# Optimization experiments

Hardware: AMD Instinct MI355X
Metric: run time of the kernel (lower is better)

The kernel has to match this reference:

```python
import jax, jax.numpy as jnp
import numpy as np

EPS = 1e-5


def setup_inputs() -> dict:
    key = jax.random.key(0)
    ks = jax.random.split(key, 8)
    B, C, D, H, O, E = 256, 64, 256, 4096, 256, 4
    x = jax.random.normal(ks[0], (B, C, D), dtype=jnp.float32)
    mask_ids = jax.random.randint(ks[1], (B, C), 0, 16)
    projection_idx = jax.random.randint(ks[2], (C,), 0, E)
    W1 = jax.random.normal(ks[3], (E, D, H), dtype=jnp.float32) * 0.02
    b1 = jnp.zeros((E, H), dtype=jnp.float32)
    gamma = jnp.ones((E, H), dtype=jnp.float32)
    beta = jnp.zeros((E, H), dtype=jnp.float32)
    W2 = jax.random.normal(ks[4], (E, H, O), dtype=jnp.float32) * 0.02
    b2 = jnp.zeros((E, O), dtype=jnp.float32)
    return {"x": x, "mask_ids": mask_ids, "projection_idx": projection_idx,
            "W1": W1, "b1": b1, "gamma": gamma, "beta": beta, "W2": W2, "b2": b2}


def reference(x, mask_ids, projection_idx, W1, b1, gamma, beta, W2, b2):
    # x: [B, C, D]; projection_idx: [C] routes each channel to one of E experts.
    # Disjoint masks => the original zeros + masked '+=' is a partition-assign.
    B, C, D = x.shape
    E, _, H = W1.shape
    # Per-channel expert params (gather once, shared over batch).
    h = jnp.einsum('bcd,cdh->bch', x, W1[projection_idx]) + b1[projection_idx]
    # BatchNorm1d in training mode: batch stats over the tokens of each expert
    # (the original flattens the selected [B, |mask|] tokens for BN).
    seg = jnp.broadcast_to(projection_idx[None, :], (B, C)).reshape(-1)  # [B*C]
    hf = h.reshape(B * C, H)
    cnt = jax.ops.segment_sum(jnp.ones((B * C,), h.dtype), seg, num_segments=E)
    cnt = jnp.maximum(cnt, 1.0)
    s1 = jax.ops.segment_sum(hf, seg, num_segments=E)            # [E, H]
    s2 = jax.ops.segment_sum(hf * hf, seg, num_segments=E)       # [E, H]
    mean = s1 / cnt[:, None]
    var = s2 / cnt[:, None] - mean * mean                        # biased var (train-mode BN)
    inv = jax.lax.rsqrt(var + EPS)
    hn = (h - mean[projection_idx]) * (inv[projection_idx] * gamma[projection_idx]) + beta[projection_idx]
    a = jax.nn.relu(hn)
    out = jnp.einsum('bch,cho->bco', a, W2[projection_idx]) + b2[projection_idx]
    return out, mask_ids
```

## Files before the change

kernel.cpp:

```cpp
#include <hip/hip_runtime.h>

typedef unsigned short u16;
typedef unsigned int   u32;
typedef __attribute__((ext_vector_type(8))) short s16x8;
typedef __attribute__((ext_vector_type(4))) float f32x4;
typedef __attribute__((ext_vector_type(4))) u32   u32x4;

#define DEV static __device__ __forceinline__

static constexpr int B_ = 256, C_ = 64, D_ = 256, H_ = 4096, O_ = 256, E_ = 4;

DEV u16 f2bf(float f) {
  u32 u = __builtin_bit_cast(u32, f);
  u += 0x7fffu + ((u >> 16) & 1u);
  return (u16)(u >> 16);
}
DEV float bf2f(u16 u) { return __builtin_bit_cast(float, (u32)u << 16); }

DEV void async16(const u16* g, u16* l) {
  __builtin_amdgcn_global_load_lds(
      (const __attribute__((address_space(1))) void*)g,
      (__attribute__((address_space(3))) void*)l, 16, 0, 0);
}

DEV int xcd_swz(int bid, int nwg) { return (bid & 7) * (nwg >> 3) + (bid >> 3); }

__global__ void k_cvt(const float* __restrict__ src, u16* __restrict__ dst) {
  const int i = blockIdx.x * blockDim.x + threadIdx.x;
  const f32x4 a = ((const f32x4*)src)[2 * i];
  const f32x4 b = ((const f32x4*)src)[2 * i + 1];
  u32x4 o;
  o[0] = (u32)f2bf(a[0]) | ((u32)f2bf(a[1]) << 16);
  o[1] = (u32)f2bf(a[2]) | ((u32)f2bf(a[3]) << 16);
  o[2] = (u32)f2bf(b[0]) | ((u32)f2bf(b[1]) << 16);
  o[3] = (u32)f2bf(b[2]) | ((u32)f2bf(b[3]) << 16);
  ((u32x4*)dst)[i] = o;
}

__global__ void k_transpose(const float* __restrict__ src, u16* __restrict__ dst,
                            const int R, const int Cc) {
  __shared__ float tile[64][65];
  const int nct = Cc >> 6, nrt = R >> 6;
  int bx = blockIdx.x;
  const int ct = bx % nct; bx /= nct;
  const int rt = bx % nrt; const int e = bx / nrt;
  const float* s = src + (size_t)e * R * Cc;
  u16* d = dst + (size_t)e * R * Cc;
  const int tx = threadIdx.x & 63, ty = threadIdx.x >> 6;
  #pragma unroll
  for (int i = 0; i < 64; i += 4)
    tile[i + ty][tx] = s[(size_t)(rt * 64 + i + ty) * Cc + ct * 64 + tx];
  __syncthreads();
  #pragma unroll
  for (int i = 0; i < 64; i += 4) {
    const int cc = i + ty;
    d[(size_t)(ct * 64 + cc) * R + rt * 64 + tx] = f2bf(tile[tx][cc]);
  }
}

__global__ void k_sortc(const int* __restrict__ proj, int* __restrict__ perm) {
  const int c = threadIdx.x;
  const int e = proj[c];
  int rank = 0;
  for (int c2 = 0; c2 < C_; ++c2) {
    const int e2 = proj[c2];
    rank += (e2 < e) || (e2 == e && c2 < c);
  }
  perm[rank] = c;
}

__global__ __launch_bounds__(256, 4)
void k_gemm1(const u16* __restrict__ A, const u16* __restrict__ Bw,
             const int* __restrict__ proj, const int* __restrict__ perm,
             const float* __restrict__ bias,
             u16* __restrict__ outH, float* __restrict__ s1g, float* __restrict__ s2g) {
  constexpr int BM = 128, BN = 128, BK = 32, KT = D_ / BK;
  constexpr int SA = BM * BK / 8, SB = BN * BK / 8;
  constexpr int BUF = (SA + SB) * 8;
  __shared__ __align__(16) u16 lds[2 * BUF];
  const int tid = threadIdx.x, l = tid & 63, w = tid >> 6, wm = w >> 1, wn = w & 1;

  int bid = xcd_swz(blockIdx.x, gridDim.x);
  constexpr int NT = H_ / BN, BT = B_ / BM;
  const int nt = bid % NT; bid /= NT;
  const int bt = bid % BT; const int ci = bid / BT;
  const int c = perm[ci];
  const int e = proj[c];

  const size_t rsA = (size_t)C_ * D_;
  const u16* Ab = A + (size_t)c * D_ + (size_t)bt * BM * rsA;
  const u16* Bb = Bw + ((size_t)e * H_ + (size_t)nt * BN) * D_;

  f32x4 acc[4][4] = {};

  auto stage = [&](int kt) {
    const int k0 = kt * BK;
    u16* dst = lds + (kt & 1) * BUF;
    #pragma unroll
    for (int i = 0; i < 2; ++i) {
      const int s = i * 256 + tid, row = s >> 2, j = (s & 3) ^ (row & 3);
      async16(Ab + (size_t)row * rsA + k0 + j * 8, dst + s * 8);
    }
    #pragma unroll
    for (int i = 0; i < 2; ++i) {
      const int s = i * 256 + tid, col = s >> 2, j = (s & 3) ^ (col & 3);
      async16(Bb + (size_t)col * D_ + k0 + j * 8, dst + SA * 8 + s * 8);
    }
  };

  stage(0);
  asm volatile("s_waitcnt vmcnt(0)" ::: "memory");
  __builtin_amdgcn_s_barrier();

  #pragma unroll
  for (int kt = 0; kt < KT; ++kt) {
    if (kt + 1 < KT) stage(kt + 1);
    const u16* bufA = lds + (kt & 1) * BUF;
    const u16* bufB = bufA + SA * 8;
    s16x8 av[4], bv[4];
    #pragma unroll
    for (int m = 0; m < 4; ++m) {
      const int r = wm * 64 + m * 16 + (l & 15), p = (l >> 4) ^ (r & 3);
      av[m] = *(const s16x8*)(bufA + (r * 4 + p) * 8);
    }
    #pragma unroll
    for (int n = 0; n < 4; ++n) {
      const int cc = wn * 64 + n * 16 + (l & 15), p = (l >> 4) ^ (cc & 3);
      bv[n] = *(const s16x8*)(bufB + (cc * 4 + p) * 8);
    }
    #pragma unroll
    for (int m = 0; m < 4; ++m)
      #pragma unroll
      for (int n = 0; n < 4; ++n)
        acc[m][n] = __builtin_amdgcn_mfma_f32_16x16x32_bf16(av[m], bv[n], acc[m][n], 0, 0, 0);
    asm volatile("s_waitcnt vmcnt(0) lgkmcnt(0)" ::: "memory");
    __builtin_amdgcn_s_barrier();
  }

  u16* ldsOut = lds;
  #pragma unroll
  for (int n = 0; n < 4; ++n) {
    const int colL = wn * 64 + n * 16 + (l & 15);
    const int colg = nt * BN + colL;
    const float bval = bias[e * H_ + colg];
    float p1 = 0.f, p2 = 0.f;
    #pragma unroll
    for (int m = 0; m < 4; ++m) {
      const int rbase = wm * 64 + m * 16 + (l >> 4) * 4;
      #pragma unroll
      for (int i = 0; i < 4; ++i) {
        const float v = acc[m][n][i] + bval;
        p1 += v; p2 += v * v;
        const int row = rbase + i;
        const int phys = (colL >> 3) ^ (row & 15);
        ldsOut[row * 128 + phys * 8 + (colL & 7)] = f2bf(v);
      }
    }
    p1 += __shfl_xor(p1, 16); p1 += __shfl_xor(p1, 32);
    p2 += __shfl_xor(p2, 16); p2 += __shfl_xor(p2, 32);
    if (l < 16) {
      atomicAdd(&s1g[e * H_ + colg], p1);
      atomicAdd(&s2g[e * H_ + colg], p2);
    }
  }
  __syncthreads();
  u16* outB = outH + ((size_t)(bt * BM) * C_ + c) * H_ + nt * BN;
  #pragma unroll
  for (int pass = 0; pass < 8; ++pass) {
    const int row = pass * 16 + (tid >> 4), sl = tid & 15;
    const u32x4 v = *(const u32x4*)(ldsOut + row * 128 + ((sl ^ (row & 15)) * 8));
    *(u32x4*)(outB + (size_t)row * C_ * H_ + sl * 8) = v;
  }
}

__global__ void k_finalize(const float* __restrict__ s1, const float* __restrict__ s2,
                           const int* __restrict__ proj, const float* __restrict__ gamma,
                           const float* __restrict__ beta,
                           u16* __restrict__ sclB, u16* __restrict__ shfB) {
  const int i = blockIdx.x * 256 + threadIdx.x;
  const int e = i >> 12;
  int cn = 0;
  #pragma unroll
  for (int c = 0; c < C_; ++c) cn += (proj[c] == e) ? 1 : 0;
  const float cnt = fmaxf((float)cn * (float)B_, 1.f);
  const float mean = s1[i] / cnt;
  const float var = s2[i] / cnt - mean * mean;
  const float sc = rsqrtf(var + 1e-5f) * gamma[i];
  sclB[i] = f2bf(sc);
  shfB[i] = f2bf(beta[i] - mean * sc);
}

__global__ __launch_bounds__(256, 2)
void k_gemm2(const u16* __restrict__ A, const u16* __restrict__ Bw,
             const int* __restrict__ proj, const int* __restrict__ perm,
             const float* __restrict__ b2,
             const u16* __restrict__ scB, const u16* __restrict__ shB,
             float* __restrict__ outF, float* __restrict__ partial) {
  constexpr int BM = 128, BN = 128, BK = 32, KH = H_ / 2, KT = KH / BK;
  constexpr int SA = BM * BK / 8, SB = BN * BK / 8;
  constexpr int BUF = (SA + SB) * 8;
  __shared__ __align__(16) u16 lds[3 * BUF + 2 * KH];
  u16* stS = lds + 3 * BUF;
  u16* stT = stS + KH;
  const int tid = threadIdx.x, l = tid & 63, w = tid >> 6, wm = w >> 1, wn = w & 1;

  int bid = xcd_swz(blockIdx.x, gridDim.x);
  const int ks = bid & 1; bid >>= 1;
  const int nt = bid & 1; bid >>= 1;
  const int bt = bid & 1; const int ci = bid >> 1;
  const int c = perm[ci];
  const int e = proj[c];

  const size_t rsA = (size_t)C_ * H_;
  const u16* Ab = A + (size_t)c * H_ + (size_t)bt * BM * rsA + (size_t)ks * KH;
  const u16* Bb = Bw + ((size_t)e * O_ + (size_t)nt * BN) * H_ + (size_t)ks * KH;
  const u16* scE = scB + e * H_ + ks * KH;
  const u16* shE = shB + e * H_ + ks * KH;

  f32x4 acc[4][4] = {};
  s16x8 h0[2], h1[2], b0r[2], b1r[2];

  auto Aissue = [&](int kt, s16x8 (&hs)[2]) {
    const int k0 = kt * BK;
    #pragma unroll
    for (int i = 0; i < 2; ++i) {
      const int s = i * 256 + tid, row = s >> 2, j = (s & 3) ^ (row & 3);
      hs[i] = *(const s16x8*)(Ab + (size_t)row * rsA + k0 + j * 8);
    }
  };
  auto Bissue = [&](int kt, s16x8 (&bs)[2]) {
    const int k0 = kt * BK;
    #pragma unroll
    for (int i = 0; i < 2; ++i) {
      const int s = i * 256 + tid, col = s >> 2, j = (s & 3) ^ (col & 3);
      bs[i] = *(const s16x8*)(Bb + (size_t)col * H_ + k0 + j * 8);
    }
  };
  auto Awrite = [&](int kt, s16x8 (&hs)[2]) {
    u16* dst = lds + (kt % 3) * BUF;
    const int k0 = kt * BK;
    #pragma unroll
    for (int i = 0; i < 2; ++i) {
      const int s = i * 256 + tid, row = s >> 2, j = (s & 3) ^ (row & 3);
      const s16x8 sv = *(const s16x8*)(stS + k0 + j * 8);
      const s16x8 tv = *(const s16x8*)(stT + k0 + j * 8);
      u32x4 o;
      #pragma unroll
      for (int jj = 0; jj < 4; ++jj) {
        const float v0 = fmaxf(bf2f((u16)hs[i][2 * jj]) * bf2f((u16)sv[2 * jj]) + bf2f((u16)tv[2 * jj]), 0.f);
        const float v1 = fmaxf(bf2f((u16)hs[i][2 * jj + 1]) * bf2f((u16)sv[2 * jj + 1]) + bf2f((u16)tv[2 * jj + 1]), 0.f);
        o[jj] = (u32)f2bf(v0) | ((u32)f2bf(v1) << 16);
      }
      *(u32x4*)(dst + s * 8) = o;
    }
  };
  auto Bwrite = [&](int kt, s16x8 (&bs)[2]) {
    u16* dst = lds + (kt % 3) * BUF + SA * 8;
    #pragma unroll
    for (int i = 0; i < 2; ++i) {
      const int s = i * 256 + tid;
      *(u32x4*)(dst + s * 8) = __builtin_bit_cast(u32x4, bs[i]);
    }
  };
  auto Compute = [&](int kt) {
    const u16* bufA = lds + (kt % 3) * BUF;
    const u16* bufB = bufA + SA * 8;
    s16x8 av[4], bv[4];
    #pragma unroll
    for (int m = 0; m < 4; ++m) {
      const int r = wm * 64 + m * 16 + (l & 15), p = (l >> 4) ^ (r & 3);
      av[m] = *(const s16x8*)(bufA + (r * 4 + p) * 8);
    }
    #pragma unroll
    for (int n = 0; n < 4; ++n) {
      const int cc = wn * 64 + n * 16 + (l & 15), p = (l >> 4) ^ (cc & 3);
      bv[n] = *(const s16x8*)(bufB + (cc * 4 + p) * 8);
    }
    #pragma unroll
    for (int m = 0; m < 4; ++m)
      #pragma unroll
      for (int n = 0; n < 4; ++n)
        acc[m][n] = __builtin_amdgcn_mfma_f32_16x16x32_bf16(av[m], bv[n], acc[m][n], 0, 0, 0);
  };

  async16(scE + tid * 8, stS + tid * 8);
  async16(shE + tid * 8, stT + tid * 8);
  Aissue(0, h0); Bissue(0, b0r);
  Aissue(1, h1); Bissue(1, b1r);
  asm volatile("s_waitcnt vmcnt(0)" ::: "memory");
  Awrite(0, h0); Bwrite(0, b0r);
  asm volatile("s_waitcnt lgkmcnt(0)" ::: "memory");
  __builtin_amdgcn_s_barrier();

  #pragma unroll 1
  for (int kt = 0; kt + 3 < KT; kt += 2) {
    Aissue(kt + 2, h0); Bissue(kt + 2, b0r);
    Awrite(kt + 1, h1); Bwrite(kt + 1, b1r);
    Compute(kt);
    asm volatile("s_waitcnt lgkmcnt(0)" ::: "memory");
    __builtin_amdgcn_s_barrier();
    Aissue(kt + 3, h1); Bissue(kt + 3, b1r);
    Awrite(kt + 2, h0); Bwrite(kt + 2, b0r);
    Compute(kt + 1);
    asm volatile("s_waitcnt lgkmcnt(0)" ::: "memory");
    __builtin_amdgcn_s_barrier();
  }

  Awrite(KT - 1, h1); Bwrite(KT - 1, b1r);
  Compute(KT - 2);
  asm volatile("s_waitcnt lgkmcnt(0)" ::: "memory");
  __builtin_amdgcn_s_barrier();
  Compute(KT - 1);

  float* dstF = ks ? partial : outF;
  #pragma unroll
  for (int n = 0; n < 4; ++n) {
    const int colg = nt * BN + wn * 64 + n * 16 + (l & 15);
    const float bval = ks ? 0.f : b2[e * O_ + colg];
    #pragma unroll
    for (int m = 0; m < 4; ++m) {
      #pragma unroll
      for (int i = 0; i < 4; ++i) {
        const int rg = bt * BM + wm * 64 + m * 16 + (l >> 4) * 4 + i;
        dstF[((size_t)rg * C_ + c) * O_ + colg] = acc[m][n][i] + bval;
      }
    }
  }
}

__global__ void k_combine(float* __restrict__ out, const float* __restrict__ partial,
                          const int* __restrict__ mask, float* __restrict__ maskOut) {
  const int gi = blockIdx.x * 256 + threadIdx.x;
  const size_t b = (size_t)gi * 2;
  f32x4 a0 = ((const f32x4*)out)[b],     a1 = ((const f32x4*)out)[b + 1];
  const f32x4 p0 = ((const f32x4*)partial)[b], p1 = ((const f32x4*)partial)[b + 1];
  #pragma unroll
  for (int j = 0; j < 4; ++j) { a0[j] += p0[j]; a1[j] += p1[j]; }
  ((f32x4*)out)[b] = a0; ((f32x4*)out)[b + 1] = a1;
  if (gi < B_ * C_ / 8) {
    #pragma unroll
    for (int j = 0; j < 8; ++j) maskOut[gi * 8 + j] = (float)mask[gi * 8 + j];
  }
}

extern "C" void kernel_launch(void* const* d_in, const int* in_sizes, int n_in,
                              void* d_out, int out_size, void* d_ws, size_t ws_size,
                              hipStream_t stream) {
  const float* x     = (const float*)d_in[0];
  const int*   mask  = (const int*)d_in[1];
  const int*   proj  = (const int*)d_in[2];
  const float* W1    = (const float*)d_in[3];
  const float* b1    = (const float*)d_in[4];
  const float* gamma = (const float*)d_in[5];
  const float* beta  = (const float*)d_in[6];
  const float* W2    = (const float*)d_in[7];
  const float* b2    = (const float*)d_in[8];
  float* out = (float*)d_out;

  char* ws = (char*)d_ws;
  size_t off = 0;
  u16* hbuf = (u16*)(ws + off); off += (size_t)B_ * C_ * H_ * 2;
  u16* xb   = (u16*)(ws + off); off += (size_t)B_ * C_ * D_ * 2;
  u16* w1t  = (u16*)(ws + off); off += (size_t)E_ * D_ * H_ * 2;
  float* partial = (float*)xb;
  u16* w2t  = (u16*)(ws + off); off += (size_t)E_ * H_ * O_ * 2;
  float* s1 = (float*)(ws + off); off += (size_t)E_ * H_ * 4;
  float* s2 = (float*)(ws + off); off += (size_t)E_ * H_ * 4;
  u16* sclB = (u16*)(ws + off); off += (size_t)E_ * H_ * 2;
  u16* shfB = (u16*)(ws + off); off += (size_t)E_ * H_ * 2;
  int* perm = (int*)(ws + off); off += 256;

  (void)hipMemsetAsync(s1, 0, (size_t)2 * E_ * H_ * 4, stream);

  k_sortc<<<1, 64, 0, stream>>>(proj, perm);
  k_cvt<<<2048, 256, 0, stream>>>(x, xb);
  k_transpose<<<E_ * 4 * 64, 256, 0, stream>>>(W1, w1t, D_, H_);
  k_transpose<<<E_ * 64 * 4, 256, 0, stream>>>(W2, w2t, H_, O_);

  k_gemm1<<<C_ * 2 * 32, 256, 0, stream>>>(xb, w1t, proj, perm, b1, hbuf, s1, s2);

  k_finalize<<<E_ * H_ / 256, 256, 0, stream>>>(s1, s2, proj, gamma, beta, sclB, shfB);

  k_gemm2<<<512, 256, 0, stream>>>(hbuf, w2t, proj, perm, b2, sclB, shfB, out, partial);

  k_combine<<<B_ * C_ * O_ / 8 / 256, 256, 0, stream>>>(out, partial, mask,
                                                        out + (size_t)B_ * C_ * O_);
}
```

Baseline: 160.1 us.

## Fuse prep kernels, split GEMM2 K four ways, double-buffer and reswizzle LDS

Merges the x conversion, both weight transposes and the channel sort into one prep launch, which removes three launches. GEMM2 gets a templated K-split. When the workspace is large enough it runs with four K slices over 1024 blocks instead of two over 512, with triple buffering cut to double buffering and launch bounds raised for occupancy. Compute is moved ahead of the LDS writes in the pipeline, and the LDS XOR swizzle changes to use row>>1 in both GEMMs. The cost is more partial-sum traffic, since the combine kernel now reads three fp32 partial buffers.

```diff
diff --git a/kernel.cpp b/kernel.cpp
--- a/kernel.cpp
+++ b/kernel.cpp
@@ -25,48 +25,57 @@
 
 DEV int xcd_swz(int bid, int nwg) { return (bid & 7) * (nwg >> 3) + (bid >> 3); }
 
-__global__ void k_cvt(const float* __restrict__ src, u16* __restrict__ dst) {
-  const int i = blockIdx.x * blockDim.x + threadIdx.x;
-  const f32x4 a = ((const f32x4*)src)[2 * i];
-  const f32x4 b = ((const f32x4*)src)[2 * i + 1];
-  u32x4 o;
-  o[0] = (u32)f2bf(a[0]) | ((u32)f2bf(a[1]) << 16);
-  o[1] = (u32)f2bf(a[2]) | ((u32)f2bf(a[3]) << 16);
-  o[2] = (u32)f2bf(b[0]) | ((u32)f2bf(b[1]) << 16);
-  o[3] = (u32)f2bf(b[2]) | ((u32)f2bf(b[3]) << 16);
-  ((u32x4*)dst)[i] = o;
-}
-
-__global__ void k_transpose(const float* __restrict__ src, u16* __restrict__ dst,
-                            const int R, const int Cc) {
+__global__ void k_prep(const float* __restrict__ x, u16* __restrict__ xb,
+                       const float* __restrict__ W1, u16* __restrict__ w1t,
+                       const float* __restrict__ W2, u16* __restrict__ w2t,
+                       const int* __restrict__ proj, int* __restrict__ perm) {
   __shared__ float tile[64][65];
-  const int nct = Cc >> 6, nrt = R >> 6;
-  int bx = blockIdx.x;
-  const int ct = bx % nct; bx /= nct;
-  const int rt = bx % nrt; const int e = bx / nrt;
-  const float* s = src + (size_t)e * R * Cc;
-  u16* d = dst + (size_t)e * R * Cc;
-  const int tx = threadIdx.x & 63, ty = threadIdx.x >> 6;
-  #pragma unroll
-  for (int i = 0; i < 64; i += 4)
-    tile[i + ty][tx] = s[(size_t)(rt * 64 + i + ty) * Cc + ct * 64 + tx];
-  __syncthreads();
-  #pragma unroll
-  for (int i = 0; i < 64; i += 4) {
-    const int cc = i + ty;
-    d[(size_t)(ct * 64 + cc) * R + rt * 64 + tx] = f2bf(tile[tx][cc]);
-  }
-}
-
-__global__ void k_sortc(const int* __restrict__ proj, int* __restrict__ perm) {
-  const int c = threadIdx.x;
-  const int e = proj[c];
-  int rank = 0;
-  for (int c2 = 0; c2 < C_; ++c2) {
-    const int e2 = proj[c2];
-    rank += (e2 < e) || (e2 == e && c2 < c);
-  }
-  perm[rank] = c;
+  const int bx = blockIdx.x, tid = threadIdx.x;
+  if (bx < 2048) {
+    const int i = bx * 256 + tid;
+    const f32x4 a = ((const f32x4*)x)[2 * i];
+    const f32x4 b = ((const f32x4*)x)[2 * i + 1];
+    u32x4 o;
+    o[0] = (u32)f2bf(a[0]) | ((u32)f2bf(a[1]) << 16);
+    o[1] = (u32)f2bf(a[2]) | ((u32)f2bf(a[3]) << 16);
+    o[2] = (u32)f2bf(b[0]) | ((u32)f2bf(b[1]) << 16);
+    o[3] = (u32)f2bf(b[2]) | ((u32)f2bf(b[3]) << 16);
+    ((u32x4*)xb)[i] = o;
+    return;
+  }
+  if (bx < 4096) {
+    const bool w1 = bx < 3072;
+    const int R  = w1 ? D_ : H_;
+    const int Cc = w1 ? H_ : O_;
+    const float* s0 = w1 ? W1 : W2;
+    u16* d0 = w1 ? w1t : w2t;
+    int b = bx - (w1 ? 2048 : 3072);
+    const int nct = Cc >> 6, nrt = R >> 6;
+    const int ct = b % nct; b /= nct;
+    const int rt = b % nrt; const int e = b / nrt;
+    const float* s = s0 + (size_t)e * R * Cc;
+    u16* d = d0 + (size_t)e * R * Cc;
+    const int tx = tid & 63, ty = tid >> 6;
+    #pragma unroll
+    for (int i = 0; i < 64; i += 4)
+      tile[i + ty][tx] = s[(size_t)(rt * 64 + i + ty) * Cc + ct * 64 + tx];
+    __syncthreads();
+    #pragma unroll
+    for (int i = 0; i < 64; i += 4) {
+      const int cc = i + ty;
+      d[(size_t)(ct * 64 + cc) * R + rt * 64 + tx] = f2bf(tile[tx][cc]);
+    }
+    return;
+  }
+  if (tid < C_) {
+    const int e = proj[tid];
+    int rank = 0;
+    for (int c2 = 0; c2 < C_; ++c2) {
+      const int e2 = proj[c2];
+      rank += (e2 < e) || (e2 == e && c2 < tid);
+    }
+    perm[rank] = tid;
+  }
 }
 
 __global__ __launch_bounds__(256, 4)
@@ -98,12 +107,12 @@
     u16* dst = lds + (kt & 1) * BUF;
     #pragma unroll
     for (int i = 0; i < 2; ++i) {
-      const int s = i * 256 + tid, row = s >> 2, j = (s & 3) ^ (row & 3);
+      const int s = i * 256 + tid, row = s >> 2, j = (s & 3) ^ ((row >> 1) & 3);
       async16(Ab + (size_t)row * rsA + k0 + j * 8, dst + s * 8);
     }
     #pragma unroll
     for (int i = 0; i < 2; ++i) {
-      const int s = i * 256 + tid, col = s >> 2, j = (s & 3) ^ (col & 3);
+      const int s = i * 256 + tid, col = s >> 2, j = (s & 3) ^ ((col >> 1) & 3);
       async16(Bb + (size_t)col * D_ + k0 + j * 8, dst + SA * 8 + s * 8);
     }
   };
@@ -120,12 +129,12 @@
     s16x8 av[4], bv[4];
     #pragma unroll
     for (int m = 0; m < 4; ++m) {
-      const int r = wm * 64 + m * 16 + (l & 15), p = (l >> 4) ^ (r & 3);
+      const int r = wm * 64 + m * 16 + (l & 15), p = (l >> 4) ^ ((r >> 1) & 3);
       av[m] = *(const s16x8*)(bufA + (r * 4 + p) * 8);
     }
     #pragma unroll
     for (int n = 0; n < 4; ++n) {
-      const int cc = wn * 64 + n * 16 + (l & 15), p = (l >> 4) ^ (cc & 3);
+      const int cc = wn * 64 + n * 16 + (l & 15), p = (l >> 4) ^ ((cc >> 1) & 3);
       bv[n] = *(const s16x8*)(bufB + (cc * 4 + p) * 8);
     }
     #pragma unroll
@@ -190,22 +199,23 @@
   shfB[i] = f2bf(beta[i] - mean * sc);
 }
 
-__global__ __launch_bounds__(256, 2)
+template<int KS>
+__global__ __launch_bounds__(256, 4)
 void k_gemm2(const u16* __restrict__ A, const u16* __restrict__ Bw,
              const int* __restrict__ proj, const int* __restrict__ perm,
              const float* __restrict__ b2,
              const u16* __restrict__ scB, const u16* __restrict__ shB,
              float* __restrict__ outF, float* __restrict__ partial) {
-  constexpr int BM = 128, BN = 128, BK = 32, KH = H_ / 2, KT = KH / BK;
+  constexpr int BM = 128, BN = 128, BK = 32, KH = H_ / KS, KT = KH / BK;
   constexpr int SA = BM * BK / 8, SB = BN * BK / 8;
   constexpr int BUF = (SA + SB) * 8;
-  __shared__ __align__(16) u16 lds[3 * BUF + 2 * KH];
-  u16* stS = lds + 3 * BUF;
+  __shared__ __align__(16) u16 lds[2 * BUF + 2 * KH];
+  u16* stS = lds + 2 * BUF;
   u16* stT = stS + KH;
   const int tid = threadIdx.x, l = tid & 63, w = tid >> 6, wm = w >> 1, wn = w & 1;
 
   int bid = xcd_swz(blockIdx.x, gridDim.x);
-  const int ks = bid & 1; bid >>= 1;
+  const int ks = bid & (KS - 1); bid /= KS;
   const int nt = bid & 1; bid >>= 1;
   const int bt = bid & 1; const int ci = bid >> 1;
   const int c = perm[ci];
@@ -224,7 +234,7 @@
     const int k0 = kt * BK;
     #pragma unroll
     for (int i = 0; i < 2; ++i) {
-      const int s = i * 256 + tid, row = s >> 2, j = (s & 3) ^ (row & 3);
+      const int s = i * 256 + tid, row = s >> 2, j = (s & 3) ^ ((row >> 1) & 3);
       hs[i] = *(const s16x8*)(Ab + (size_t)row * rsA + k0 + j * 8);
     }
   };
@@ -232,16 +242,16 @@
     const int k0 = kt * BK;
     #pragma unroll
     for (int i = 0; i < 2; ++i) {
-      const int s = i * 256 + tid, col = s >> 2, j = (s & 3) ^ (col & 3);
+      const int s = i * 256 + tid, col = s >> 2, j = (s & 3) ^ ((col >> 1) & 3);
       bs[i] = *(const s16x8*)(Bb + (size_t)col * H_ + k0 + j * 8);
     }
   };
   auto Awrite = [&](int kt, s16x8 (&hs)[2]) {
-    u16* dst = lds + (kt % 3) * BUF;
+    u16* dst = lds + (kt & 1) * BUF;
     const int k0 = kt * BK;
     #pragma unroll
     for (int i = 0; i < 2; ++i) {
-      const int s = i * 256 + tid, row = s >> 2, j = (s & 3) ^ (row & 3);
+      const int s = i * 256 + tid, row = s >> 2, j = (s & 3) ^ ((row >> 1) & 3);
       const s16x8 sv = *(const s16x8*)(stS + k0 + j * 8);
       const s16x8 tv = *(const s16x8*)(stT + k0 + j * 8);
       u32x4 o;
@@ -255,7 +265,7 @@
     }
   };
   auto Bwrite = [&](int kt, s16x8 (&bs)[2]) {
-    u16* dst = lds + (kt % 3) * BUF + SA * 8;
+    u16* dst = lds + (kt & 1) * BUF + SA * 8;
     #pragma unroll
     for (int i = 0; i < 2; ++i) {
       const int s = i * 256 + tid;
@@ -263,17 +273,17 @@
     }
   };
   auto Compute = [&](int kt) {
-    const u16* bufA = lds + (kt % 3) * BUF;
+    const u16* bufA = lds + (kt & 1) * BUF;
     const u16* bufB = bufA + SA * 8;
     s16x8 av[4], bv[4];
     #pragma unroll
     for (int m = 0; m < 4; ++m) {
-      const int r = wm * 64 + m * 16 + (l & 15), p = (l >> 4) ^ (r & 3);
+      const int r = wm * 64 + m * 16 + (l & 15), p = (l >> 4) ^ ((r >> 1) & 3);
       av[m] = *(const s16x8*)(bufA + (r * 4 + p) * 8);
     }
     #pragma unroll
     for (int n = 0; n < 4; ++n) {
-      const int cc = wn * 64 + n * 16 + (l & 15), p = (l >> 4) ^ (cc & 3);
+      const int cc = wn * 64 + n * 16 + (l & 15), p = (l >> 4) ^ ((cc >> 1) & 3);
       bv[n] = *(const s16x8*)(bufB + (cc * 4 + p) * 8);
     }
     #pragma unroll
@@ -283,11 +293,14 @@
         acc[m][n] = __builtin_amdgcn_mfma_f32_16x16x32_bf16(av[m], bv[n], acc[m][n], 0, 0, 0);
   };
 
-  async16(scE + tid * 8, stS + tid * 8);
-  async16(shE + tid * 8, stT + tid * 8);
+  for (int q = tid; q < KH / 4; q += 256) {
+    if (q < KH / 8) async16(scE + q * 8, stS + q * 8);
+    else            async16(shE + (q - KH / 8) * 8, stT + (q - KH / 8) * 8);
+  }
   Aissue(0, h0); Bissue(0, b0r);
   Aissue(1, h1); Bissue(1, b1r);
   asm volatile("s_waitcnt vmcnt(0)" ::: "memory");
+  __builtin_amdgcn_s_barrier();
   Awrite(0, h0); Bwrite(0, b0r);
   asm volatile("s_waitcnt lgkmcnt(0)" ::: "memory");
   __builtin_amdgcn_s_barrier();
@@ -295,24 +308,24 @@
   #pragma unroll 1
   for (int kt = 0; kt + 3 < KT; kt += 2) {
     Aissue(kt + 2, h0); Bissue(kt + 2, b0r);
+    Compute(kt);
     Awrite(kt + 1, h1); Bwrite(kt + 1, b1r);
-    Compute(kt);
     asm volatile("s_waitcnt lgkmcnt(0)" ::: "memory");
     __builtin_amdgcn_s_barrier();
     Aissue(kt + 3, h1); Bissue(kt + 3, b1r);
+    Compute(kt + 1);
     Awrite(kt + 2, h0); Bwrite(kt + 2, b0r);
-    Compute(kt + 1);
     asm volatile("s_waitcnt lgkmcnt(0)" ::: "memory");
     __builtin_amdgcn_s_barrier();
   }
 
+  Compute(KT - 2);
   Awrite(KT - 1, h1); Bwrite(KT - 1, b1r);
-  Compute(KT - 2);
   asm volatile("s_waitcnt lgkmcnt(0)" ::: "memory");
   __builtin_amdgcn_s_barrier();
   Compute(KT - 1);
 
-  float* dstF = ks ? partial : outF;
+  float* dstF = ks ? (partial + (size_t)(ks - 1) * B_ * C_ * O_) : outF;
   #pragma unroll
   for (int n = 0; n < 4; ++n) {
     const int colg = nt * BN + wn * 64 + n * 16 + (l & 15);
@@ -329,13 +342,18 @@
 }
 
 __global__ void k_combine(float* __restrict__ out, const float* __restrict__ partial,
-                          const int* __restrict__ mask, float* __restrict__ maskOut) {
+                          const int nparts, const int* __restrict__ mask,
+                          float* __restrict__ maskOut) {
   const int gi = blockIdx.x * 256 + threadIdx.x;
   const size_t b = (size_t)gi * 2;
-  f32x4 a0 = ((const f32x4*)out)[b],     a1 = ((const f32x4*)out)[b + 1];
-  const f32x4 p0 = ((const f32x4*)partial)[b], p1 = ((const f32x4*)partial)[b + 1];
-  #pragma unroll
-  for (int j = 0; j < 4; ++j) { a0[j] += p0[j]; a1[j] += p1[j]; }
+  constexpr size_t PARTV = (size_t)B_ * C_ * O_ / 4;
+  f32x4 a0 = ((const f32x4*)out)[b], a1 = ((const f32x4*)out)[b + 1];
+  for (int p = 0; p < nparts; ++p) {
+    const f32x4 p0 = ((const f32x4*)partial)[p * PARTV + b];
+    const f32x4 p1 = ((const f32x4*)partial)[p * PARTV + b + 1];
+    #pragma unroll
+    for (int j = 0; j < 4; ++j) { a0[j] += p0[j]; a1[j] += p1[j]; }
+  }
   ((f32x4*)out)[b] = a0; ((f32x4*)out)[b + 1] = a1;
   if (gi < B_ * C_ / 8) {
     #pragma unroll
@@ -362,27 +380,32 @@
   u16* hbuf = (u16*)(ws + off); off += (size_t)B_ * C_ * H_ * 2;
   u16* xb   = (u16*)(ws + off); off += (size_t)B_ * C_ * D_ * 2;
   u16* w1t  = (u16*)(ws + off); off += (size_t)E_ * D_ * H_ * 2;
-  float* partial = (float*)xb;
+  float* partial2 = (float*)xb;
   u16* w2t  = (u16*)(ws + off); off += (size_t)E_ * H_ * O_ * 2;
   float* s1 = (float*)(ws + off); off += (size_t)E_ * H_ * 4;
   float* s2 = (float*)(ws + off); off += (size_t)E_ * H_ * 4;
   u16* sclB = (u16*)(ws + off); off += (size_t)E_ * H_ * 2;
   u16* shfB = (u16*)(ws + off); off += (size_t)E_ * H_ * 2;
   int* perm = (int*)(ws + off); off += 256;
+  off = (off + 255) & ~(size_t)255;
+  float* partial4 = (float*)(ws + off);
+  const bool ks4 = ws_size >= off + (size_t)3 * B_ * C_ * O_ * 4;
 
   (void)hipMemsetAsync(s1, 0, (size_t)2 * E_ * H_ * 4, stream);
 
-  k_sortc<<<1, 64, 0, stream>>>(proj, perm);
-  k_cvt<<<2048, 256, 0, stream>>>(x, xb);
-  k_transpose<<<E_ * 4 * 64, 256, 0, stream>>>(W1, w1t, D_, H_);
-  k_transpose<<<E_ * 64 * 4, 256, 0, stream>>>(W2, w2t, H_, O_);
+  k_prep<<<4097, 256, 0, stream>>>(x, xb, W1, w1t, W2, w2t, proj, perm);
 
   k_gemm1<<<C_ * 2 * 32, 256, 0, stream>>>(xb, w1t, proj, perm, b1, hbuf, s1, s2);
 
   k_finalize<<<E_ * H_ / 256, 256, 0, stream>>>(s1, s2, proj, gamma, beta, sclB, shfB);
 
-  k_gemm2<<<512, 256, 0, stream>>>(hbuf, w2t, proj, perm, b2, sclB, shfB, out, partial);
-
-  k_combine<<<B_ * C_ * O_ / 8 / 256, 256, 0, stream>>>(out, partial, mask,
-                                                        out + (size_t)B_ * C_ * O_);
-}
+  if (ks4) {
+    k_gemm2<4><<<1024, 256, 0, stream>>>(hbuf, w2t, proj, perm, b2, sclB, shfB, out, partial4);
+    k_combine<<<B_ * C_ * O_ / 8 / 256, 256, 0, stream>>>(out, partial4, 3, mask,
+                                                          out + (size_t)B_ * C_ * O_);
+  } else {
+    k_gemm2<2><<<512, 256, 0, stream>>>(hbuf, w2t, proj, perm, b2, sclB, shfB, out, partial2);
+    k_combine<<<B_ * C_ * O_ / 8 / 256, 256, 0, stream>>>(out, partial2, 1, mask,
+                                                          out + (size_t)B_ * C_ * O_);
+  }
+}
```

Result: slower. 183.0 us (+14.3%).
